# Optimization experiments

Hardware: AMD Instinct MI355X
Metric: run time of the kernel (lower is better)

The kernel has to match this reference:

```python
import jax, jax.numpy as jnp
import numpy as np

D_MODEL, D_STATE, EXPAND = 1024, 128, 2
E = D_MODEL * EXPAND          # 2048
N = D_STATE                   # 128
H = 1
P = E
TD = D_STATE // 2             # 64
Z_DIM = E + E + N + N + H + H + TD + H  # 4369
EPS = 1e-05
B_SZ, L = 4, 2048


def setup_inputs() -> dict:
    key = jax.random.key(0)
    ks = jax.random.split(key, 6)
    u = jax.random.normal(ks[0], (B_SZ, L, D_MODEL), dtype=jnp.float32)
    W_in = jax.random.normal(ks[1], (Z_DIM, D_MODEL), dtype=jnp.float32) * 0.02
    W_out = jax.random.normal(ks[2], (D_MODEL, E), dtype=jnp.float32) * 0.02
    w_normB = jnp.ones((N,), jnp.float32)
    w_normC = jnp.ones((N,), jnp.float32)
    B_bias = jnp.ones((N,), jnp.float32)
    C_bias = jnp.ones((N,), jnp.float32)
    # dt_bias buffer: dt_i ~ logU(0.001, 0.1); dt_bias = dt_i + log(-expm1(-dt_i))
    dt_i = jnp.exp(jax.random.uniform(ks[3], (H,)) * (np.log(0.1) - np.log(0.001)) + np.log(0.001))
    dt_i = jnp.clip(dt_i, 1e-4, None)
    dt_bias = dt_i + jnp.log(-jnp.expm1(-dt_i))
    A_log = jnp.full((H,), np.log(0.5), jnp.float32)
    return {"u": u, "W_in": W_in, "w_normB": w_normB, "w_normC": w_normC,
            "B_bias": B_bias, "C_bias": C_bias, "dt_bias": dt_bias,
            "A_log": A_log, "W_out": W_out}


def _rms(x, w):
    return x * jax.lax.rsqrt(jnp.mean(x * x, axis=-1, keepdims=True) + EPS) * w


def _rope(x, ang):
    half = x.shape[-1] // 2
    x1, x2 = x[..., :half], x[..., half:]
    c, s = jnp.cos(ang), jnp.sin(ang)
    return jnp.concatenate([x1 * c - x2 * s, x1 * s + x2 * c], axis=-1)


def reference(u, W_in, w_normB, w_normC, B_bias, C_bias, dt_bias, A_log, W_out):
    Bb, Ls, _ = u.shape
    z = u @ W_in.T  # [B, L, Z_DIM]
    o = 0
    def take(n):
        nonlocal o
        r = z[..., o:o + n]; o += n; return r
    x = jax.nn.silu(take(E))
    gate = jax.nn.silu(take(E))
    B_ = take(N)
    C_ = take(N)
    dt_ = take(H)
    A_ = take(H)
    th = take(TD)
    lam_ = take(H)

    dt = jax.nn.softplus(dt_ + dt_bias)          # [B, L, H]
    A = -jax.nn.softplus(A_ + A_log)             # [B, L, H]
    lam = jax.nn.sigmoid(lam_)                   # [B, L, H]
    alpha = jnp.exp(dt * A)                      # [B, L, H]

    B_ = _rms(B_, w_normB) + B_bias
    C_ = _rms(C_, w_normC) + C_bias
    ca = jnp.cumsum(jnp.mean(dt, axis=-1, keepdims=True) * th, axis=1)  # [B, L, TD]
    B_ = _rope(B_, ca)
    C_ = _rope(C_, ca)

    xh = x.reshape(Bb, Ls, H, P)
    xp = jnp.concatenate([jnp.zeros_like(xh[:, :1]), xh[:, :-1]], axis=1)  # roll + zero t=0
    lh = lam[..., None]
    xt = lh * xh + (1.0 - lh) * alpha[..., None] * xp  # [B, L, H, P]

    # fallback SSM: per-channel mean drive, per-head scalar A (mean over batch+time)
    u_mean = jnp.mean(xt, axis=-1)               # [B, L, H]
    A_bar = jnp.mean(A, axis=(0, 1))             # [H]
    dA = jnp.exp(dt * A_bar)                     # [B, L, H]
    dBu = dt[..., None] * B_[:, :, None, :] * u_mean[..., None]  # [B, L, H, N]

    def step(state, xs):
        dA_t, dBu_t, C_t = xs                    # [B,H], [B,H,N], [B,N]
        state = dA_t[..., None] * state + dBu_t  # [B, H, N]
        y_t = jnp.einsum('bhn,bn->bh', state, C_t)
        return state, y_t

    state0 = jnp.zeros((Bb, H, N), dtype=xt.dtype)
    _, ys = jax.lax.scan(step, state0,
                         (jnp.moveaxis(dA, 1, 0), jnp.moveaxis(dBu, 1, 0), jnp.moveaxis(C_, 1, 0)))
    outs = jnp.moveaxis(ys, 0, 1)                # [B, L, H]
    y = jnp.broadcast_to(outs, (Bb, Ls, E))      # H=1 expanded to E
    return (y * gate) @ W_out.T
```

## Files before the change

### kernel.cpp

```cpp
#include <hip/hip_runtime.h>
#include <cstdint>
#include <cstddef>

typedef __bf16 bf16_t;
typedef bf16_t bf16x8 __attribute__((ext_vector_type(8)));
typedef float f32x4 __attribute__((ext_vector_type(4)));

#define B_SZ    4
#define LSEQ    2048
#define DMODEL  1024
#define EDIM    2048
#define ZDIM    4419
#define ZPAD    4608
#define ROWS    (B_SZ*LSEQ)
#define EPSV    1e-5f

#define LDU     1088
#define LDG     2112

#define SCHUNK  128
#define SCLEN   (LSEQ/SCHUNK)
#define RCH     128
#define RCLEN   (LSEQ/RCH)

__device__ __forceinline__ float softplus_f(float x){
  return fmaxf(x, 0.f) + log1pf(expf(-fabsf(x)));
}
__device__ __forceinline__ float sigmoid_f(float x){ return 1.f/(1.f+expf(-x)); }
__device__ __forceinline__ float silu_f(float x){ return x/(1.f+expf(-x)); }

__device__ __forceinline__ void gload_lds16(const void* g, void* l){
  __builtin_amdgcn_global_load_lds(
      (const __attribute__((address_space(1))) void*)g,
      (__attribute__((address_space(3))) void*)l, 16, 0, 0);
}

__device__ __forceinline__ float blockReduce128(float v, float* red, int t){
  red[t] = v; __syncthreads();
  #pragma unroll
  for (int off = 64; off > 0; off >>= 1){
    if (t < off) red[t] += red[t+off];
    __syncthreads();
  }
  float r = red[0];
  __syncthreads();
  return r;
}

__global__ __launch_bounds__(256) void prep_kernel(
    const float* __restrict__ u, const float* __restrict__ win, const float* __restrict__ wout,
    bf16_t* __restrict__ ubf, bf16_t* __restrict__ winbf, bf16_t* __restrict__ woutbf,
    float* __restrict__ Asum, float* __restrict__ xraw)
{
  size_t i = (size_t)blockIdx.x*256 + threadIdx.x;
  if (i == 0) Asum[0] = 0.f;
  if (i < ROWS) xraw[i] = 0.f;
  const size_t NU = (size_t)ROWS*DMODEL;
  const size_t NW = (size_t)ZPAD*DMODEL;
  const size_t NO = (size_t)DMODEL*EDIM;
  if (i < NU){
    size_t row = i >> 10, col = i & 1023;
    ubf[row*LDU + col] = (bf16_t)u[i];
    return;
  }
  i -= NU;
  if (i < NW){
    size_t row = i >> 10, col = i & 1023;
    winbf[row*LDU + col] = (row < (size_t)ZDIM) ? (bf16_t)win[i] : (bf16_t)0.f;
    return;
  }
  i -= NW;
  if (i < NO){
    size_t row = i >> 11, col = i & 2047;
    woutbf[row*LDG + col] = (bf16_t)wout[i];
  }
}

template<int BM, int NT, int NXT, int MODE>
__global__ __launch_bounds__(512, 2) void gemmP_kernel(
    const bf16_t* __restrict__ A, const int lda,
    const bf16_t* __restrict__ W, const int ldw,
    float* __restrict__ xraw, bf16_t* __restrict__ o_g, float* __restrict__ o_z,
    const float* __restrict__ scale, float* __restrict__ o_f)
{
  constexpr int BN = 256;
  constexpr int MR = BM/32;
  constexpr int BUFE = (BM+BN)*64;
  __shared__ __align__(16) bf16_t lds[BUFE*3];

  const int tid = threadIdx.x;
  const int wid = tid>>6, lane = tid&63;
  const int wr = wid>>2, wc = wid&3;
  const int lr = lane&15;

  const int nwg = NXT*(ROWS/BM);
  const int id = blockIdx.x;
  const int rid = (id & 7)*(nwg>>3) + (id>>3);
  const int bx = rid % NXT, by = rid / NXT;
  const int m0 = by*BM, n0 = bx*BN;

  f32x4 acc[MR][4] = {};

  auto stageA = [&](int buf, int t){
    bf16_t* lA = lds + buf*BUFE;
    const int k0 = t*64;
    #pragma unroll
    for (int q = 0; q < BM/64; ++q){
      int cidx = q*512 + tid;
      int row = cidx>>3, sc = (cidx&7) ^ (row&7);
      gload_lds16(A + (size_t)(m0+row)*lda + k0 + sc*8,
                  lA + (size_t)(q*512 + wid*64)*8);
    }
  };
  auto stageB = [&](int buf, int t){
    bf16_t* lB = lds + buf*BUFE + BM*64;
    const int k0 = t*64;
    #pragma unroll
    for (int q = 0; q < 4; ++q){
      int cidx = q*512 + tid;
      int row = cidx>>3, sc = (cidx&7) ^ (row&7);
      gload_lds16(W + (size_t)(n0+row)*ldw + k0 + sc*8,
                  lB + (size_t)(q*512 + wid*64)*8);
    }
  };
  auto dsread = [&](int buf, int kk, bf16x8* af, bf16x8* bfr){
    const bf16_t* lA = lds + buf*BUFE;
    const bf16_t* lB = lA + BM*64;
    const int g = kk*4 + (lane>>4);
    #pragma unroll
    for (int n = 0; n < 4; ++n){
      int rr = wc*64 + n*16 + lr;
      bfr[n] = *(const bf16x8*)&lB[rr*64 + ((g^(rr&7))<<3)];
    }
    #pragma unroll
    for (int m = 0; m < MR; ++m){
      int rr = wr*(BM/2) + m*16 + lr;
      af[m] = *(const bf16x8*)&lA[rr*64 + ((g^(rr&7))<<3)];
    }
  };
  auto domfma = [&](bf16x8* af, bf16x8* bfr){
    asm volatile("s_waitcnt lgkmcnt(0)" ::: "memory");
    __builtin_amdgcn_sched_barrier(0);
    __builtin_amdgcn_s_setprio(1);
    #pragma unroll
    for (int m = 0; m < MR; ++m)
      #pragma unroll
      for (int n = 0; n < 4; ++n)
        acc[m][n] = __builtin_amdgcn_mfma_f32_16x16x32_bf16(af[m], bfr[n], acc[m][n], 0,0,0);
    __builtin_amdgcn_s_setprio(0);
  };

  stageA(0,0); stageB(0,0);
  stageA(1,1); stageB(1,1);
  int cur = 0;
  for (int t = 0; t < NT; ++t){
    int nb = cur+2; if (nb >= 3) nb -= 3;
    const bool st = (t+2 < NT);
    if (st){
      stageA(nb, t+2);
      asm volatile("s_waitcnt vmcnt(8)" ::: "memory");
    } else if (t+1 < NT){
      asm volatile("s_waitcnt vmcnt(6)" ::: "memory");
    } else {
      asm volatile("s_waitcnt vmcnt(0)" ::: "memory");
    }
    asm volatile("s_barrier" ::: "memory");
    {
      bf16x8 af[MR], bfr[4];
      dsread(cur, 0, af, bfr);
      domfma(af, bfr);
    }
    asm volatile("s_barrier" ::: "memory");
    {
      bf16x8 af[MR], bfr[4];
      dsread(cur, 1, af, bfr);
      if (st) stageB(nb, t+2);
      domfma(af, bfr);
    }
    asm volatile("s_barrier" ::: "memory");
    if (++cur == 3) cur = 0;
  }

  if (MODE == 0 && n0 < 2048){
    #pragma unroll
    for (int m = 0; m < MR; ++m){
      #pragma unroll
      for (int i = 0; i < 4; ++i){
        float p = 0.f;
        #pragma unroll
        for (int n = 0; n < 4; ++n) p += silu_f(acc[m][n][i]);
        #pragma unroll
        for (int off = 8; off > 0; off >>= 1) p += __shfl_xor(p, off);
        if (lr == 0){
          int r = m0 + wr*(BM/2) + m*16 + ((lane>>4)<<2) + i;
          atomicAdd(xraw + r, p);
        }
      }
    }
  } else {
    #pragma unroll
    for (int m = 0; m < MR; ++m){
      int rowb = m0 + wr*(BM/2) + m*16 + ((lane>>4)<<2);
      #pragma unroll
      for (int n = 0; n < 4; ++n){
        int col = n0 + wc*64 + n*16 + lr;
        #pragma unroll
        for (int i = 0; i < 4; ++i){
          int r = rowb + i;
          float v = acc[m][n][i];
          if (MODE == 0){
            if (col < 4096)      o_g[(size_t)r*LDG + (col-2048)] = (bf16_t)silu_f(v);
            else if (col < 4480) o_z[(size_t)r*384 + (col-4096)] = v;
          } else {
            o_f[(size_t)r*DMODEL + col] = v * scale[r];
          }
        }
      }
    }
  }
}

__global__ __launch_bounds__(128) void fuse_kernel(
    const float* __restrict__ xraw, const float* __restrict__ zs,
    const float* __restrict__ wnB, const float* __restrict__ wnC,
    const float* __restrict__ Bb, const float* __restrict__ Cb,
    const float* __restrict__ dtb, const float* __restrict__ Alog,
    float* __restrict__ Bn, float* __restrict__ Cn, float* __restrict__ dtth,
    float* __restrict__ dts, float* __restrict__ alphas, float* __restrict__ lams,
    float* __restrict__ xbar, float* Asum)
{
  __shared__ float red[128];
  int r = blockIdx.x, t = threadIdx.x;
  const float* zr = zs + (size_t)r*384;
  float bv = zr[t], cv = zr[128+t];
  float b2 = blockReduce128(bv*bv, red, t);
  float c2 = blockReduce128(cv*cv, red, t);
  float rb = rsqrtf(b2*(1.f/128.f) + EPSV);
  float rc = rsqrtf(c2*(1.f/128.f) + EPSV);
  Bn[(size_t)r*128 + t] = bv*rb*wnB[t] + Bb[t];
  Cn[(size_t)r*128 + t] = cv*rc*wnC[t] + Cb[t];

  float dt = softplus_f(zr[256] + dtb[0]);
  if (t < 64) dtth[(size_t)r*64 + t] = dt * zr[258+t];
  if (t == 0){
    float Av  = -softplus_f(zr[257] + Alog[0]);
    float lam = sigmoid_f(zr[322]);
    dts[r]    = dt;
    alphas[r] = expf(dt*Av);
    lams[r]   = lam;
    xbar[r]   = xraw[r] * (1.f/2048.f);
    atomicAdd(Asum, Av);
  }
}

__global__ __launch_bounds__(64) void rope_sum_kernel(
    const float* __restrict__ dtth, float* __restrict__ csum)
{
  int b  = blockIdx.x >> 7;
  int ch = blockIdx.x & 127;
  int d  = threadIdx.x;
  const float* base = dtth + ((size_t)b*LSEQ + (size_t)ch*RCLEN)*64 + d;
  float s = 0.f;
  #pragma unroll
  for (int i = 0; i < RCLEN; ++i) s += base[(size_t)i*64];
  csum[((size_t)b*RCH + ch)*64 + d] = s;
}

__global__ __launch_bounds__(64) void rope_prefix_kernel(float* __restrict__ csum)
{
  int b = blockIdx.x, d = threadIdx.x;
  float s = 0.f;
  for (int c = 0; c < RCH; ++c){
    size_t idx = ((size_t)b*RCH + c)*64 + d;
    float v = csum[idx]; csum[idx] = s; s += v;
  }
}

__global__ __launch_bounds__(64) void rope_apply_kernel(
    const float* __restrict__ dtth, const float* __restrict__ csum,
    float* __restrict__ Bn, float* __restrict__ Cn)
{
  int b  = blockIdx.x >> 7;
  int ch = blockIdx.x & 127;
  int d  = threadIdx.x;
  float ca = csum[((size_t)b*RCH + ch)*64 + d];
  int l0 = ch*RCLEN;
  const float* base = dtth + ((size_t)b*LSEQ)*64 + d;
  for (int l = l0; l < l0 + RCLEN; ++l){
    ca += base[(size_t)l*64];
    float sn, cs;
    sincosf(ca, &sn, &cs);
    size_t ro = ((size_t)b*LSEQ + l)*128;
    float b1 = Bn[ro+d], b2v = Bn[ro+64+d];
    Bn[ro+d]    = b1*cs - b2v*sn;
    Bn[ro+64+d] = b1*sn + b2v*cs;
    float c1 = Cn[ro+d], c2v = Cn[ro+64+d];
    Cn[ro+d]    = c1*cs - c2v*sn;
    Cn[ro+64+d] = c1*sn + c2v*cs;
  }
}

__global__ __launch_bounds__(64) void scan_local_kernel(
    const float* __restrict__ dts, const float* __restrict__ alphas,
    const float* __restrict__ lams, const float* __restrict__ xbar,
    const float* __restrict__ Asum,
    const float* __restrict__ Bn, const float* __restrict__ Cn,
    float* __restrict__ ylocal, float* __restrict__ Pfix,
    float* __restrict__ Sfin, float* __restrict__ Dch)
{
  int b  = blockIdx.x / SCHUNK;
  int ch = blockIdx.x % SCHUNK;
  int n  = threadIdx.x;
  float Abar = Asum[0] * (1.f/(float)ROWS);
  float s1 = 0.f, s2 = 0.f, P = 1.f;
  int l0 = ch*SCLEN;
  #pragma unroll
  for (int i = 0; i < SCLEN; ++i){
    int l = l0 + i;
    size_t r = (size_t)b*LSEQ + l;
    float dt = dts[r], lam = lams[r], al = alphas[r], xb = xbar[r];
    float xp = (l > 0) ? xbar[r-1] : 0.f;
    float um = lam*xb + (1.f-lam)*al*xp;
    float dA = expf(dt*Abar);
    float coef = dt*um;
    size_t ro = r*128;
    s1 = dA*s1 + coef*Bn[ro+n];
    s2 = dA*s2 + coef*Bn[ro+64+n];
    P *= dA;
    float p = s1*Cn[ro+n] + s2*Cn[ro+64+n];
    #pragma unroll
    for (int off = 32; off > 0; off >>= 1) p += __shfl_down(p, off);
    if (n == 0){ ylocal[r] = p; Pfix[r] = P; }
  }
  size_t so = ((size_t)b*SCHUNK + ch)*128;
  Sfin[so + n]      = s1;
  Sfin[so + 64 + n] = s2;
  if (n == 0) Dch[b*SCHUNK + ch] = P;
}

__global__ __launch_bounds__(128) void scan_carry_kernel(
    const float* __restrict__ Sfin, const float* __restrict__ Dch,
    float* __restrict__ Sin)
{
  int b = blockIdx.x;
  int n = threadIdx.x;
  float s = 0.f;
  for (int c = 0; c < SCHUNK; ++c){
    size_t so = ((size_t)b*SCHUNK + c)*128;
    Sin[so + n] = s;
    s = Dch[b*SCHUNK + c]*s + Sfin[so + n];
  }
}

__global__ __launch_bounds__(256) void scan_fix_kernel(
    const float* __restrict__ Cn, const float* __restrict__ Sin,
    const float* __restrict__ ylocal, const float* __restrict__ Pfix,
    float* __restrict__ outsv)
{
  int r = blockIdx.x*4 + (threadIdx.x>>6);
  int n = threadIdx.x & 63;
  int b  = r / LSEQ;
  int ch = (r % LSEQ) / SCLEN;
  const float* si = Sin + ((size_t)b*SCHUNK + ch)*128;
  size_t ro = (size_t)r*128;
  float p = Cn[ro+n]*si[n] + Cn[ro+64+n]*si[64+n];
  #pragma unroll
  for (int off = 32; off > 0; off >>= 1) p += __shfl_down(p, off);
  if (n == 0) outsv[r] = ylocal[r] + Pfix[r]*p;
}

extern "C" void kernel_launch(void* const* d_in, const int* in_sizes, int n_in,
                              void* d_out, int out_size, void* d_ws, size_t ws_size,
                              hipStream_t stream)
{
  const float* u    = (const float*)d_in[0];
  const float* W_in = (const float*)d_in[1];
  const float* wnB  = (const float*)d_in[2];
  const float* wnC  = (const float*)d_in[3];
  const float* Bb   = (const float*)d_in[4];
  const float* Cb   = (const float*)d_in[5];
  const float* dtb  = (const float*)d_in[6];
  const float* Alog = (const float*)d_in[7];
  const float* Wout = (const float*)d_in[8];
  float* out = (float*)d_out;
  char* ws = (char*)d_ws;

  constexpr size_t OFF_ASUM = 0;
  constexpr size_t OFF_UBF  = 256;
  constexpr size_t SZ_UBF   = (size_t)ROWS*LDU*2;
  constexpr size_t OFF_WIN  = OFF_UBF + SZ_UBF;
  constexpr size_t SZ_WIN   = (size_t)ZPAD*LDU*2;
  constexpr size_t OFF_WOUT = OFF_WIN + SZ_WIN;
  constexpr size_t SZ_WOUT  = (size_t)DMODEL*LDG*2;
  constexpr size_t OFF_G    = OFF_WOUT + SZ_WOUT;
  constexpr size_t SZ_G     = (size_t)ROWS*LDG*2;
  constexpr size_t OFF_ZS   = OFF_G + SZ_G;
  constexpr size_t SZ_ZS    = (size_t)ROWS*384*4;
  constexpr size_t OFF_BN   = OFF_ZS + SZ_ZS;
  constexpr size_t SZ_BN    = (size_t)ROWS*128*4;
  constexpr size_t OFF_CN   = OFF_BN + SZ_BN;
  constexpr size_t OFF_DTTH = OFF_CN + SZ_BN;
  constexpr size_t SZ_DTTH  = (size_t)ROWS*64*4;
  constexpr size_t OFF_XRAW = OFF_DTTH + SZ_DTTH;
  constexpr size_t OFF_DT   = OFF_XRAW + (size_t)ROWS*4;
  constexpr size_t OFF_AL   = OFF_DT  + (size_t)ROWS*4;
  constexpr size_t OFF_LAM  = OFF_AL  + (size_t)ROWS*4;
  constexpr size_t OFF_XB   = OFF_LAM + (size_t)ROWS*4;
  constexpr size_t OFF_OUTS = OFF_XB  + (size_t)ROWS*4;
  constexpr size_t OFF_YLOC = OFF_OUTS + (size_t)ROWS*4;
  constexpr size_t OFF_PFIX = OFF_YLOC + (size_t)ROWS*4;
  constexpr size_t OFF_SFIN = OFF_PFIX + (size_t)ROWS*4;
  constexpr size_t SZ_SFIN  = (size_t)B_SZ*SCHUNK*128*4;
  constexpr size_t OFF_DCH  = OFF_SFIN + SZ_SFIN;
  constexpr size_t OFF_SIN  = OFF_DCH + (size_t)B_SZ*SCHUNK*4;
  constexpr size_t OFF_CSUM = OFF_SIN + SZ_SFIN;

  float*  Asum   = (float*) (ws + OFF_ASUM);
  bf16_t* ubf    = (bf16_t*)(ws + OFF_UBF);
  bf16_t* winbf  = (bf16_t*)(ws + OFF_WIN);
  bf16_t* woutbf = (bf16_t*)(ws + OFF_WOUT);
  bf16_t* gbuf   = (bf16_t*)(ws + OFF_G);
  float*  zsb    = (float*) (ws + OFF_ZS);
  float*  Bn     = (float*) (ws + OFF_BN);
  float*  Cn     = (float*) (ws + OFF_CN);
  float*  dtth   = (float*) (ws + OFF_DTTH);
  float*  xraw   = (float*) (ws + OFF_XRAW);
  float*  dts    = (float*) (ws + OFF_DT);
  float*  alphas = (float*) (ws + OFF_AL);
  float*  lams   = (float*) (ws + OFF_LAM);
  float*  xbar   = (float*) (ws + OFF_XB);
  float*  outsv  = (float*) (ws + OFF_OUTS);
  float*  ylocal = (float*) (ws + OFF_YLOC);
  float*  Pfix   = (float*) (ws + OFF_PFIX);
  float*  Sfin   = (float*) (ws + OFF_SFIN);
  float*  Dch    = (float*) (ws + OFF_DCH);
  float*  Sin    = (float*) (ws + OFF_SIN);
  float*  csum   = (float*) (ws + OFF_CSUM);

  {
    size_t total = (size_t)ROWS*DMODEL + (size_t)ZPAD*DMODEL + (size_t)DMODEL*EDIM;
    int blocks = (int)((total + 255)/256);
    prep_kernel<<<blocks, 256, 0, stream>>>(u, W_in, Wout, ubf, winbf, woutbf, Asum, xraw);
  }
  gemmP_kernel<128, DMODEL/64, ZPAD/256, 0><<<(ZPAD/256)*(ROWS/128), 512, 0, stream>>>(
      ubf, LDU, winbf, LDU, xraw, gbuf, zsb, nullptr, nullptr);
  fuse_kernel<<<ROWS, 128, 0, stream>>>(xraw, zsb, wnB, wnC, Bb, Cb, dtb, Alog,
                                        Bn, Cn, dtth, dts, alphas, lams, xbar, Asum);
  rope_sum_kernel<<<B_SZ*RCH, 64, 0, stream>>>(dtth, csum);
  rope_prefix_kernel<<<B_SZ, 64, 0, stream>>>(csum);
  rope_apply_kernel<<<B_SZ*RCH, 64, 0, stream>>>(dtth, csum, Bn, Cn);
  scan_local_kernel<<<B_SZ*SCHUNK, 64, 0, stream>>>(dts, alphas, lams, xbar, Asum,
                                                    Bn, Cn, ylocal, Pfix, Sfin, Dch);
  scan_carry_kernel<<<B_SZ, 128, 0, stream>>>(Sfin, Dch, Sin);
  scan_fix_kernel<<<ROWS/4, 256, 0, stream>>>(Cn, Sin, ylocal, Pfix, outsv);
  gemmP_kernel<128, EDIM/64, DMODEL/256, 1><<<(DMODEL/256)*(ROWS/128), 512, 0, stream>>>(
      gbuf, LDG, woutbf, LDG, nullptr, nullptr, nullptr, outsv, out);
}
```

Baseline: 332.8 us.

## Enlarge GEMM tiles with double buffering and vectorize prep conversion

The templated GEMM takes configurable tile and warp-layout parameters. The input projection moves to 256x256 tiles and the output projection to 256x128 tiles. The triple-buffered pipeline becomes a double-buffered one with a single prefetch stage and one fewer barrier per k-step, and the fp32-to-bf16 prep kernel now handles four elements per thread with float4 loads. Larger tiles raise data reuse and cut global traffic, but they use more registers per thread and launch fewer workgroups, which lowers occupancy and the ability to hide latency.

```diff
diff --git a/kernel.cpp b/kernel.cpp
--- a/kernel.cpp
+++ b/kernel.cpp
@@ -4,6 +4,7 @@
 
 typedef __bf16 bf16_t;
 typedef bf16_t bf16x8 __attribute__((ext_vector_type(8)));
+typedef bf16_t bf16x4 __attribute__((ext_vector_type(4)));
 typedef float f32x4 __attribute__((ext_vector_type(4)));
 
 #define B_SZ    4
@@ -48,49 +49,63 @@
 }
 
 __global__ __launch_bounds__(256) void prep_kernel(
-    const float* __restrict__ u, const float* __restrict__ win, const float* __restrict__ wout,
+    const float4* __restrict__ u4, const float4* __restrict__ win4,
+    const float4* __restrict__ wout4,
     bf16_t* __restrict__ ubf, bf16_t* __restrict__ winbf, bf16_t* __restrict__ woutbf,
     float* __restrict__ Asum, float* __restrict__ xraw)
 {
   size_t i = (size_t)blockIdx.x*256 + threadIdx.x;
   if (i == 0) Asum[0] = 0.f;
   if (i < ROWS) xraw[i] = 0.f;
-  const size_t NU = (size_t)ROWS*DMODEL;
-  const size_t NW = (size_t)ZPAD*DMODEL;
-  const size_t NO = (size_t)DMODEL*EDIM;
-  if (i < NU){
-    size_t row = i >> 10, col = i & 1023;
-    ubf[row*LDU + col] = (bf16_t)u[i];
+  const size_t NU4 = (size_t)ROWS*DMODEL/4;
+  const size_t NW4 = (size_t)ZPAD*DMODEL/4;
+  const size_t NO4 = (size_t)DMODEL*EDIM/4;
+  if (i < NU4){
+    float4 v = u4[i];
+    size_t e = i*4, row = e>>10, col = e&1023;
+    bf16x4 o = { (bf16_t)v.x, (bf16_t)v.y, (bf16_t)v.z, (bf16_t)v.w };
+    *(bf16x4*)&ubf[row*LDU + col] = o;
     return;
   }
-  i -= NU;
-  if (i < NW){
-    size_t row = i >> 10, col = i & 1023;
-    winbf[row*LDU + col] = (row < (size_t)ZDIM) ? (bf16_t)win[i] : (bf16_t)0.f;
+  i -= NU4;
+  if (i < NW4){
+    size_t e = i*4, row = e>>10, col = e&1023;
+    bf16x4 o;
+    if (row < (size_t)ZDIM){
+      float4 v = win4[i];
+      o = bf16x4{ (bf16_t)v.x, (bf16_t)v.y, (bf16_t)v.z, (bf16_t)v.w };
+    } else {
+      o = bf16x4{ (bf16_t)0.f, (bf16_t)0.f, (bf16_t)0.f, (bf16_t)0.f };
+    }
+    *(bf16x4*)&winbf[row*LDU + col] = o;
     return;
   }
-  i -= NW;
-  if (i < NO){
-    size_t row = i >> 11, col = i & 2047;
-    woutbf[row*LDG + col] = (bf16_t)wout[i];
-  }
-}
-
-template<int BM, int NT, int NXT, int MODE>
-__global__ __launch_bounds__(512, 2) void gemmP_kernel(
+  i -= NW4;
+  if (i < NO4){
+    float4 v = wout4[i];
+    size_t e = i*4, row = e>>11, col = e&2047;
+    bf16x4 o = { (bf16_t)v.x, (bf16_t)v.y, (bf16_t)v.z, (bf16_t)v.w };
+    *(bf16x4*)&woutbf[row*LDG + col] = o;
+  }
+}
+
+template<int BM, int BN, int WM, int WN, int NT, int NXT, int MODE>
+__global__ __launch_bounds__(512, 2) void gemmQ_kernel(
     const bf16_t* __restrict__ A, const int lda,
     const bf16_t* __restrict__ W, const int ldw,
     float* __restrict__ xraw, bf16_t* __restrict__ o_g, float* __restrict__ o_z,
     const float* __restrict__ scale, float* __restrict__ o_f)
 {
-  constexpr int BN = 256;
-  constexpr int MR = BM/32;
+  constexpr int MR = BM/WM/16;
+  constexpr int NR = BN/WN/16;
+  constexpr int LA = BM/64;
+  constexpr int LB = BN/64;
   constexpr int BUFE = (BM+BN)*64;
-  __shared__ __align__(16) bf16_t lds[BUFE*3];
+  __shared__ __align__(16) bf16_t lds[BUFE*2];
 
   const int tid = threadIdx.x;
   const int wid = tid>>6, lane = tid&63;
-  const int wr = wid>>2, wc = wid&3;
+  const int wr = wid / WN, wc = wid % WN;
   const int lr = lane&15;
 
   const int nwg = NXT*(ROWS/BM);
@@ -99,13 +114,13 @@
   const int bx = rid % NXT, by = rid / NXT;
   const int m0 = by*BM, n0 = bx*BN;
 
-  f32x4 acc[MR][4] = {};
+  f32x4 acc[MR][NR] = {};
 
   auto stageA = [&](int buf, int t){
     bf16_t* lA = lds + buf*BUFE;
     const int k0 = t*64;
     #pragma unroll
-    for (int q = 0; q < BM/64; ++q){
+    for (int q = 0; q < LA; ++q){
       int cidx = q*512 + tid;
       int row = cidx>>3, sc = (cidx&7) ^ (row&7);
       gload_lds16(A + (size_t)(m0+row)*lda + k0 + sc*8,
@@ -116,69 +131,55 @@
     bf16_t* lB = lds + buf*BUFE + BM*64;
     const int k0 = t*64;
     #pragma unroll
-    for (int q = 0; q < 4; ++q){
+    for (int q = 0; q < LB; ++q){
       int cidx = q*512 + tid;
       int row = cidx>>3, sc = (cidx&7) ^ (row&7);
       gload_lds16(W + (size_t)(n0+row)*ldw + k0 + sc*8,
                   lB + (size_t)(q*512 + wid*64)*8);
     }
   };
-  auto dsread = [&](int buf, int kk, bf16x8* af, bf16x8* bfr){
+  auto phase = [&](int buf, int kk){
     const bf16_t* lA = lds + buf*BUFE;
     const bf16_t* lB = lA + BM*64;
     const int g = kk*4 + (lane>>4);
-    #pragma unroll
-    for (int n = 0; n < 4; ++n){
-      int rr = wc*64 + n*16 + lr;
+    bf16x8 af[MR], bfr[NR];
+    #pragma unroll
+    for (int n = 0; n < NR; ++n){
+      int rr = wc*(BN/WN) + n*16 + lr;
       bfr[n] = *(const bf16x8*)&lB[rr*64 + ((g^(rr&7))<<3)];
     }
     #pragma unroll
     for (int m = 0; m < MR; ++m){
-      int rr = wr*(BM/2) + m*16 + lr;
+      int rr = wr*(BM/WM) + m*16 + lr;
       af[m] = *(const bf16x8*)&lA[rr*64 + ((g^(rr&7))<<3)];
     }
-  };
-  auto domfma = [&](bf16x8* af, bf16x8* bfr){
     asm volatile("s_waitcnt lgkmcnt(0)" ::: "memory");
     __builtin_amdgcn_sched_barrier(0);
     __builtin_amdgcn_s_setprio(1);
     #pragma unroll
     for (int m = 0; m < MR; ++m)
       #pragma unroll
-      for (int n = 0; n < 4; ++n)
+      for (int n = 0; n < NR; ++n)
         acc[m][n] = __builtin_amdgcn_mfma_f32_16x16x32_bf16(af[m], bfr[n], acc[m][n], 0,0,0);
     __builtin_amdgcn_s_setprio(0);
   };
 
-  stageA(0,0); stageB(0,0);
-  stageA(1,1); stageB(1,1);
+  stageA(0, 0); stageB(0, 0);
   int cur = 0;
   for (int t = 0; t < NT; ++t){
-    int nb = cur+2; if (nb >= 3) nb -= 3;
-    const bool st = (t+2 < NT);
-    if (st){
-      stageA(nb, t+2);
-      asm volatile("s_waitcnt vmcnt(8)" ::: "memory");
-    } else if (t+1 < NT){
-      asm volatile("s_waitcnt vmcnt(6)" ::: "memory");
+    const bool pf = (t+1 < NT);
+    if (pf){
+      stageA(cur^1, t+1);
+      asm volatile("s_waitcnt vmcnt(4)" ::: "memory");
     } else {
       asm volatile("s_waitcnt vmcnt(0)" ::: "memory");
     }
     asm volatile("s_barrier" ::: "memory");
-    {
-      bf16x8 af[MR], bfr[4];
-      dsread(cur, 0, af, bfr);
-      domfma(af, bfr);
-    }
+    phase(cur, 0);
+    if (pf) stageB(cur^1, t+1);
+    phase(cur, 1);
     asm volatile("s_barrier" ::: "memory");
-    {
-      bf16x8 af[MR], bfr[4];
-      dsread(cur, 1, af, bfr);
-      if (st) stageB(nb, t+2);
-      domfma(af, bfr);
-    }
-    asm volatile("s_barrier" ::: "memory");
-    if (++cur == 3) cur = 0;
+    cur ^= 1;
   }
 
   if (MODE == 0 && n0 < 2048){
@@ -188,11 +189,11 @@
       for (int i = 0; i < 4; ++i){
         float p = 0.f;
         #pragma unroll
-        for (int n = 0; n < 4; ++n) p += silu_f(acc[m][n][i]);
+        for (int n = 0; n < NR; ++n) p += silu_f(acc[m][n][i]);
         #pragma unroll
         for (int off = 8; off > 0; off >>= 1) p += __shfl_xor(p, off);
         if (lr == 0){
-          int r = m0 + wr*(BM/2) + m*16 + ((lane>>4)<<2) + i;
+          int r = m0 + wr*(BM/WM) + m*16 + ((lane>>4)<<2) + i;
           atomicAdd(xraw + r, p);
         }
       }
@@ -200,10 +201,10 @@
   } else {
     #pragma unroll
     for (int m = 0; m < MR; ++m){
-      int rowb = m0 + wr*(BM/2) + m*16 + ((lane>>4)<<2);
+      int rowb = m0 + wr*(BM/WM) + m*16 + ((lane>>4)<<2);
       #pragma unroll
-      for (int n = 0; n < 4; ++n){
-        int col = n0 + wc*64 + n*16 + lr;
+      for (int n = 0; n < NR; ++n){
+        int col = n0 + wc*(BN/WN) + n*16 + lr;
         #pragma unroll
         for (int i = 0; i < 4; ++i){
           int r = rowb + i;
@@ -438,11 +439,14 @@
   float*  csum   = (float*) (ws + OFF_CSUM);
 
   {
-    size_t total = (size_t)ROWS*DMODEL + (size_t)ZPAD*DMODEL + (size_t)DMODEL*EDIM;
-    int blocks = (int)((total + 255)/256);
-    prep_kernel<<<blocks, 256, 0, stream>>>(u, W_in, Wout, ubf, winbf, woutbf, Asum, xraw);
-  }
-  gemmP_kernel<128, DMODEL/64, ZPAD/256, 0><<<(ZPAD/256)*(ROWS/128), 512, 0, stream>>>(
+    size_t total4 = ((size_t)ROWS*DMODEL + (size_t)ZPAD*DMODEL + (size_t)DMODEL*EDIM)/4;
+    int blocks = (int)((total4 + 255)/256);
+    prep_kernel<<<blocks, 256, 0, stream>>>(
+        (const float4*)u, (const float4*)W_in, (const float4*)Wout,
+        ubf, winbf, woutbf, Asum, xraw);
+  }
+  gemmQ_kernel<256, 256, 2, 4, DMODEL/64, ZPAD/256, 0>
+      <<<(ZPAD/256)*(ROWS/256), 512, 0, stream>>>(
       ubf, LDU, winbf, LDU, xraw, gbuf, zsb, nullptr, nullptr);
   fuse_kernel<<<ROWS, 128, 0, stream>>>(xraw, zsb, wnB, wnC, Bb, Cb, dtb, Alog,
                                         Bn, Cn, dtth, dts, alphas, lams, xbar, Asum);
@@ -453,6 +457,7 @@
                                                     Bn, Cn, ylocal, Pfix, Sfin, Dch);
   scan_carry_kernel<<<B_SZ, 128, 0, stream>>>(Sfin, Dch, Sin);
   scan_fix_kernel<<<ROWS/4, 256, 0, stream>>>(Cn, Sin, ylocal, Pfix, outsv);
-  gemmP_kernel<128, EDIM/64, DMODEL/256, 1><<<(DMODEL/256)*(ROWS/128), 512, 0, stream>>>(
+  gemmQ_kernel<256, 128, 4, 2, EDIM/64, DMODEL/128, 1>
+      <<<(DMODEL/128)*(ROWS/256), 512, 0, stream>>>(
       gbuf, LDG, woutbf, LDG, nullptr, nullptr, nullptr, outsv, out);
 }
```

New measurement: 323.0 us. 1.03x faster.
